# Kernel tuning notes

Measured on AMD Instinct MI355X. Metric: run time of the kernel, lower is better.

The kernel has to match this reference:

```python
import jax, jax.numpy as jnp
import numpy as np

B, N, F_IN, D = 4, 2048, 32, 64  # D = output_dim; gat1: heads=4, d=D//2=32; gat2: heads=1, d=D


def _gat(x, adj_norm, Wq, bq, Wk, bk, Wv, bv, heads, d):
    b, n, _ = x.shape
    q = (x @ Wq + bq).reshape(b, n, heads, d)
    k = (x @ Wk + bk).reshape(b, n, heads, d)
    v = (x @ Wv + bv).reshape(b, n, heads, d)
    scores = jnp.einsum('bihd,bjhd->bhij', q, k) / jnp.sqrt(jnp.float32(d))
    mask = jnp.where(adj_norm == 0, jnp.float32(-1e9), jnp.float32(0.0))  # [N,N]
    w = jax.nn.softmax(scores + mask[None, None], axis=-1)
    out = jnp.einsum('bhij,bjhd->bihd', w, v)
    return out.reshape(b, n, heads * d)


def setup_inputs() -> dict:
    key = jax.random.key(0)
    ks = jax.random.split(key, 12)
    s = 0.05
    x = jax.random.normal(ks[0], (B, N, F_IN), dtype=jnp.float32)
    adj = (jax.random.uniform(ks[1], (N, N)) < 0.02).astype(jnp.float32)  # sparse binary graph
    return {
        'x': x, 'adj': adj,
        'Wp': jax.random.normal(ks[2], (F_IN, D)) * s, 'bp': jnp.zeros((D,), jnp.float32),
        'Wq1': jax.random.normal(ks[3], (F_IN, 2 * D)) * s, 'bq1': jnp.zeros((2 * D,), jnp.float32),
        'Wk1': jax.random.normal(ks[4], (F_IN, 2 * D)) * s, 'bk1': jnp.zeros((2 * D,), jnp.float32),
        'Wv1': jax.random.normal(ks[5], (F_IN, 2 * D)) * s, 'bv1': jnp.zeros((2 * D,), jnp.float32),
        'Wq2': jax.random.normal(ks[6], (2 * D, D)) * s, 'bq2': jnp.zeros((D,), jnp.float32),
        'Wk2': jax.random.normal(ks[7], (2 * D, D)) * s, 'bk2': jnp.zeros((D,), jnp.float32),
        'Wv2': jax.random.normal(ks[8], (2 * D, D)) * s, 'bv2': jnp.zeros((D,), jnp.float32),
        'gamma': jnp.ones((D,), jnp.float32), 'beta': jnp.zeros((D,), jnp.float32),
    }


def reference(x, adj, Wp, bp, Wq1, bq1, Wk1, bk1, Wv1, bv1,
              Wq2, bq2, Wk2, bk2, Wv2, bv2, gamma, beta):
    # row-normalized adjacency (normalize_adjacency)
    adj_n = adj / (jnp.sum(adj, axis=1, keepdims=True) + 1e-6)
    proj = x @ Wp + bp                                   # [B,N,D]
    h = _gat(x, adj_n, Wq1, bq1, Wk1, bk1, Wv1, bv1, 4, D // 2)   # [B,N,2D]
    h = jax.nn.relu(h)                                   # dropout inactive (training=False)
    h = _gat(h, adj_n, Wq2, bq2, Wk2, bk2, Wv2, bv2, 1, D)        # [B,N,D]
    y = h + proj
    mu = jnp.mean(y, axis=-1, keepdims=True)
    var = jnp.var(y, axis=-1, keepdims=True)
    return gamma * (y - mu) / jnp.sqrt(var + 1e-6) + beta
```

## Files before the change

### kernel.cpp

```cpp
#include <hip/hip_runtime.h>
#include <hip/hip_bf16.h>

#define BB 4
#define NN 2048
#define FIN 32
#define DD 64
#define MAXDEG 256

__device__ __forceinline__ float bflo(unsigned u) { return __uint_as_float(u << 16); }
__device__ __forceinline__ float bfhi(unsigned u) { return __uint_as_float(u & 0xffff0000u); }
__device__ __forceinline__ float bf1(unsigned short s) { return __uint_as_float((unsigned)s << 16); }
__device__ __forceinline__ unsigned short f2bf(float f) {
    union { float f; unsigned u; } x; x.f = f;
    const unsigned r = x.u + 0x7fffu + ((x.u >> 16) & 1u);
    return (unsigned short)(r >> 16);
}

__global__ __launch_bounds__(128) void csr_gemm1(const float* __restrict__ adj,
    int* __restrict__ deg, int* __restrict__ col,
    const float* __restrict__ x,
    const float* __restrict__ Wp, const float* __restrict__ bp,
    const float* __restrict__ Wq, const float* __restrict__ bq,
    const float* __restrict__ Wk, const float* __restrict__ bk,
    const float* __restrict__ Wv, const float* __restrict__ bv,
    float* __restrict__ proj, float* __restrict__ q1,
    unsigned short* __restrict__ k1, unsigned short* __restrict__ v1) {
    const int bid = blockIdx.x;
    const int tid = threadIdx.x;

    if (bid < NN / 2) {
        const int lane = tid & 63;
        const int i = bid * 2 + (tid >> 6);
        const unsigned long long below = (1ull << lane) - 1ull;
        int base = 0;
        for (int j0 = 0; j0 < NN; j0 += 256) {
            const float4 a = *(const float4*)(adj + (size_t)i * NN + j0 + lane * 4);
            const bool n0 = a.x != 0.0f, n1 = a.y != 0.0f, n2 = a.z != 0.0f, n3 = a.w != 0.0f;
            const unsigned long long m0 = __ballot(n0);
            const unsigned long long m1 = __ballot(n1);
            const unsigned long long m2 = __ballot(n2);
            const unsigned long long m3 = __ballot(n3);
            int slot = base + __popcll(m0 & below) + __popcll(m1 & below)
                            + __popcll(m2 & below) + __popcll(m3 & below);
            const int jb = j0 + 4 * lane;
            if (n0) { if (slot < MAXDEG) col[i * MAXDEG + slot] = jb;     ++slot; }
            if (n1) { if (slot < MAXDEG) col[i * MAXDEG + slot] = jb + 1; ++slot; }
            if (n2) { if (slot < MAXDEG) col[i * MAXDEG + slot] = jb + 2; ++slot; }
            if (n3) { if (slot < MAXDEG) col[i * MAXDEG + slot] = jb + 3; ++slot; }
            base += __popcll(m0) + __popcll(m1) + __popcll(m2) + __popcll(m3);
        }
        if (lane == 0) deg[i] = base < MAXDEG ? base : MAXDEG;
        return;
    }

    const int r0 = (bid - NN / 2) * 4;
    __shared__ float xs[FIN * 4];
    {
        const int r = tid >> 5, k = tid & 31;
        xs[k * 4 + r] = x[(size_t)r0 * FIN + tid];
    }
    __syncthreads();

    float aq0 = bq[tid], aq1 = aq0, aq2 = aq0, aq3 = aq0;
    float ak0 = bk[tid], ak1 = ak0, ak2 = ak0, ak3 = ak0;
    float av0 = bv[tid], av1 = av0, av2 = av0, av3 = av0;
    #pragma unroll
    for (int k = 0; k < FIN; ++k) {
        const float wq = Wq[k * 128 + tid];
        const float wk = Wk[k * 128 + tid];
        const float wv = Wv[k * 128 + tid];
        const float4 xv = *(const float4*)&xs[k * 4];
        aq0 = fmaf(xv.x, wq, aq0); aq1 = fmaf(xv.y, wq, aq1);
        aq2 = fmaf(xv.z, wq, aq2); aq3 = fmaf(xv.w, wq, aq3);
        ak0 = fmaf(xv.x, wk, ak0); ak1 = fmaf(xv.y, wk, ak1);
        ak2 = fmaf(xv.z, wk, ak2); ak3 = fmaf(xv.w, wk, ak3);
        av0 = fmaf(xv.x, wv, av0); av1 = fmaf(xv.y, wv, av1);
        av2 = fmaf(xv.z, wv, av2); av3 = fmaf(xv.w, wv, av3);
    }
    q1[(size_t)(r0 + 0) * 128 + tid] = aq0; q1[(size_t)(r0 + 1) * 128 + tid] = aq1;
    q1[(size_t)(r0 + 2) * 128 + tid] = aq2; q1[(size_t)(r0 + 3) * 128 + tid] = aq3;
    k1[(size_t)(r0 + 0) * 128 + tid] = f2bf(ak0); k1[(size_t)(r0 + 1) * 128 + tid] = f2bf(ak1);
    k1[(size_t)(r0 + 2) * 128 + tid] = f2bf(ak2); k1[(size_t)(r0 + 3) * 128 + tid] = f2bf(ak3);
    v1[(size_t)(r0 + 0) * 128 + tid] = f2bf(av0); v1[(size_t)(r0 + 1) * 128 + tid] = f2bf(av1);
    v1[(size_t)(r0 + 2) * 128 + tid] = f2bf(av2); v1[(size_t)(r0 + 3) * 128 + tid] = f2bf(av3);

    if (tid < 64) {
        float a0 = bp[tid], a1 = a0, a2 = a0, a3 = a0;
        #pragma unroll
        for (int k = 0; k < FIN; ++k) {
            const float wp = Wp[k * 64 + tid];
            const float4 xv = *(const float4*)&xs[k * 4];
            a0 = fmaf(xv.x, wp, a0); a1 = fmaf(xv.y, wp, a1);
            a2 = fmaf(xv.z, wp, a2); a3 = fmaf(xv.w, wp, a3);
        }
        proj[(size_t)(r0 + 0) * 64 + tid] = a0; proj[(size_t)(r0 + 1) * 64 + tid] = a1;
        proj[(size_t)(r0 + 2) * 64 + tid] = a2; proj[(size_t)(r0 + 3) * 64 + tid] = a3;
    }
}

__global__ __launch_bounds__(192) void gemm2_fused(const unsigned short* __restrict__ h,
    const float* __restrict__ Wq, const float* __restrict__ bq,
    const float* __restrict__ Wk, const float* __restrict__ bk,
    const float* __restrict__ Wv, const float* __restrict__ bv,
    float* __restrict__ q2, unsigned short* __restrict__ k2,
    unsigned short* __restrict__ v2) {
    const int r0 = blockIdx.x * 8;
    const int tid = threadIdx.x;
    const int mat = tid / 64;
    const int c = tid & 63;
    __shared__ float xs[128][8];
    for (int idx = tid; idx < 8 * 128; idx += 192) {
        const int r = idx >> 7, k = idx & 127;
        xs[k][r] = bf1(h[(size_t)r0 * 128 + idx]);
    }
    __syncthreads();

    const float* __restrict__ W   = mat == 0 ? Wq : (mat == 1 ? Wk : Wv);
    const float* __restrict__ bia = mat == 0 ? bq : (mat == 1 ? bk : bv);

    float acc[8];
    const float b0 = bia[c];
    #pragma unroll
    for (int r = 0; r < 8; ++r) acc[r] = b0;
    #pragma unroll 4
    for (int k = 0; k < 128; ++k) {
        const float w = W[(size_t)k * 64 + c];
        const float4 xa = *(const float4*)&xs[k][0];
        const float4 xb = *(const float4*)&xs[k][4];
        acc[0] = fmaf(xa.x, w, acc[0]); acc[1] = fmaf(xa.y, w, acc[1]);
        acc[2] = fmaf(xa.z, w, acc[2]); acc[3] = fmaf(xa.w, w, acc[3]);
        acc[4] = fmaf(xb.x, w, acc[4]); acc[5] = fmaf(xb.y, w, acc[5]);
        acc[6] = fmaf(xb.z, w, acc[6]); acc[7] = fmaf(xb.w, w, acc[7]);
    }
    if (mat == 0) {
        #pragma unroll
        for (int r = 0; r < 8; ++r) q2[(size_t)(r0 + r) * 64 + c] = acc[r];
    } else {
        unsigned short* __restrict__ Yb = mat == 1 ? k2 : v2;
        #pragma unroll
        for (int r = 0; r < 8; ++r) Yb[(size_t)(r0 + r) * 64 + c] = f2bf(acc[r]);
    }
}

__device__ __forceinline__ void map_bi(int bid, int& b, int& i) {
    const int xcd = bid & 7;
    const int w = bid >> 3;
    b = xcd & 3;
    i = ((xcd >> 2) << 10) | w;
}

__global__ __launch_bounds__(128) void attn1_relu(const float* __restrict__ q1,
                                                  const unsigned short* __restrict__ k1,
                                                  const unsigned short* __restrict__ v1,
                                                  const int* __restrict__ deg,
                                                  const int* __restrict__ col,
                                                  unsigned short* __restrict__ h) {
    int b, i;
    map_bi(blockIdx.x, b, i);
    const int tid = threadIdx.x;

    __shared__ int nbr[MAXDEG];
    __shared__ float qs[128];
    __shared__ float ws[4 * MAXDEG];
    __shared__ int sdeg;

    const size_t stride = (size_t)NN * 128;
    if (tid == 0) sdeg = deg[i];
    qs[tid] = q1[(size_t)b * stride + (size_t)i * 128 + tid];
    __syncthreads();
    const int d = sdeg;
    for (int s = tid; s < d; s += 128) nbr[s] = col[i * MAXDEG + s];
    __syncthreads();

    const float scale = 0.17677669529663687f;
    const int hh = tid >> 5;
    const int t  = tid & 31;
    const int nr = (d + 31) >> 5;

    float qf[32];
    #pragma unroll
    for (int kk = 0; kk < 32; ++kk) qf[kk] = qs[hh * 32 + kk];

    float sc[8];
    for (int r = 0; r < nr; ++r) {
        const int idx = r * 32 + t;
        float s = -INFINITY;
        if (idx < d) {
            const int j = nbr[idx];
            const unsigned short* kr = k1 + (size_t)b * stride + (size_t)j * 128 + hh * 32;
            const uint4* kr4 = (const uint4*)kr;
            float acc0 = 0.0f, acc1 = 0.0f;
            #pragma unroll
            for (int w = 0; w < 4; w += 2) {
                const uint4 ka = kr4[w];
                const uint4 kb = kr4[w + 1];
                const float* qa = &qf[w * 8];
                const float* qb = &qf[w * 8 + 8];
                acc0 = fmaf(qa[0], bflo(ka.x), acc0); acc0 = fmaf(qa[1], bfhi(ka.x), acc0);
                acc0 = fmaf(qa[2], bflo(ka.y), acc0); acc0 = fmaf(qa[3], bfhi(ka.y), acc0);
                acc0 = fmaf(qa[4], bflo(ka.z), acc0); acc0 = fmaf(qa[5], bfhi(ka.z), acc0);
                acc0 = fmaf(qa[6], bflo(ka.w), acc0); acc0 = fmaf(qa[7], bfhi(ka.w), acc0);
                acc1 = fmaf(qb[0], bflo(kb.x), acc1); acc1 = fmaf(qb[1], bfhi(kb.x), acc1);
                acc1 = fmaf(qb[2], bflo(kb.y), acc1); acc1 = fmaf(qb[3], bfhi(kb.y), acc1);
                acc1 = fmaf(qb[4], bflo(kb.z), acc1); acc1 = fmaf(qb[5], bfhi(kb.z), acc1);
                acc1 = fmaf(qb[6], bflo(kb.w), acc1); acc1 = fmaf(qb[7], bfhi(kb.w), acc1);
            }
            s = (acc0 + acc1) * scale;
        }
        sc[r] = s;
    }

    float mx = sc[0];
    for (int r = 1; r < nr; ++r) mx = fmaxf(mx, sc[r]);
    #pragma unroll
    for (int off = 16; off >= 1; off >>= 1) mx = fmaxf(mx, __shfl_xor(mx, off));
    float se = 0.0f;
    for (int r = 0; r < nr; ++r) {
        const float e = __expf(sc[r] - mx);
        sc[r] = e;
        se += e;
    }
    #pragma unroll
    for (int off = 16; off >= 1; off >>= 1) se += __shfl_xor(se, off);
    const float inv = (d > 0) ? 1.0f / se : 0.0f;
    for (int r = 0; r < nr; ++r) {
        const int idx = r * 32 + t;
        if (idx < d) ws[hh * MAXDEG + idx] = sc[r] * inv;
    }
    __syncthreads();

    const int c = tid;
    const int h2 = c >> 5;
    const unsigned short* __restrict__ vb = v1 + (size_t)b * stride + c;
    const float* __restrict__ wp = ws + h2 * MAXDEG;
    float a0 = 0.0f, a1 = 0.0f, a2 = 0.0f, a3 = 0.0f;
    int t2 = 0;
    for (; t2 + 4 <= d; t2 += 4) {
        const int j0 = nbr[t2], j1 = nbr[t2 + 1], j2 = nbr[t2 + 2], j3 = nbr[t2 + 3];
        a0 = fmaf(wp[t2 + 0], bf1(vb[(size_t)j0 * 128]), a0);
        a1 = fmaf(wp[t2 + 1], bf1(vb[(size_t)j1 * 128]), a1);
        a2 = fmaf(wp[t2 + 2], bf1(vb[(size_t)j2 * 128]), a2);
        a3 = fmaf(wp[t2 + 3], bf1(vb[(size_t)j3 * 128]), a3);
    }
    for (; t2 < d; ++t2) a0 = fmaf(wp[t2], bf1(vb[(size_t)nbr[t2] * 128]), a0);
    float o = (a0 + a1) + (a2 + a3);
    if (d == 0) {
        float a = 0.0f;
        for (int j = 0; j < NN; ++j) a += bf1(vb[(size_t)j * 128]);
        o = a * (1.0f / NN);
    }
    h[(size_t)b * stride + (size_t)i * 128 + c] = f2bf(fmaxf(o, 0.0f));
}

__global__ __launch_bounds__(64) void attn2_ln(const float* __restrict__ q2,
                                               const unsigned short* __restrict__ k2,
                                               const unsigned short* __restrict__ v2,
                                               const float* __restrict__ proj,
                                               const int* __restrict__ deg,
                                               const int* __restrict__ col,
                                               const float* __restrict__ gamma,
                                               const float* __restrict__ beta,
                                               float* __restrict__ out) {
    int b, i;
    map_bi(blockIdx.x, b, i);
    const int lane = threadIdx.x;

    __shared__ int nbr[MAXDEG];
    __shared__ float qs[64];
    __shared__ float ws[MAXDEG];
    __shared__ int sdeg;

    const size_t stride = (size_t)NN * 64;
    if (lane == 0) sdeg = deg[i];
    qs[lane] = q2[(size_t)b * stride + (size_t)i * 64 + lane];
    __syncthreads();
    const int d = sdeg;
    for (int s = lane; s < d; s += 64) nbr[s] = col[i * MAXDEG + s];
    __syncthreads();

    const float scale = 0.125f;
    const int nr = (d + 63) >> 6;

    float sc[4];
    for (int r = 0; r < nr; ++r) {
        const int idx = r * 64 + lane;
        float s = -INFINITY;
        if (idx < d) {
            const int j = nbr[idx];
            const uint4* kr4 = (const uint4*)(k2 + (size_t)b * stride + (size_t)j * 64);
            float acc0 = 0.0f, acc1 = 0.0f;
            #pragma unroll
            for (int w = 0; w < 8; w += 2) {
                const uint4 ka = kr4[w];
                const uint4 kb = kr4[w + 1];
                const float4 qa0 = *(const float4*)&qs[w * 8];
                const float4 qa1 = *(const float4*)&qs[w * 8 + 4];
                const float4 qb0 = *(const float4*)&qs[w * 8 + 8];
                const float4 qb1 = *(const float4*)&qs[w * 8 + 12];
                acc0 = fmaf(qa0.x, bflo(ka.x), acc0); acc0 = fmaf(qa0.y, bfhi(ka.x), acc0);
                acc0 = fmaf(qa0.z, bflo(ka.y), acc0); acc0 = fmaf(qa0.w, bfhi(ka.y), acc0);
                acc0 = fmaf(qa1.x, bflo(ka.z), acc0); acc0 = fmaf(qa1.y, bfhi(ka.z), acc0);
                acc0 = fmaf(qa1.z, bflo(ka.w), acc0); acc0 = fmaf(qa1.w, bfhi(ka.w), acc0);
                acc1 = fmaf(qb0.x, bflo(kb.x), acc1); acc1 = fmaf(qb0.y, bfhi(kb.x), acc1);
                acc1 = fmaf(qb0.z, bflo(kb.y), acc1); acc1 = fmaf(qb0.w, bfhi(kb.y), acc1);
                acc1 = fmaf(qb1.x, bflo(kb.z), acc1); acc1 = fmaf(qb1.y, bfhi(kb.z), acc1);
                acc1 = fmaf(qb1.z, bflo(kb.w), acc1); acc1 = fmaf(qb1.w, bfhi(kb.w), acc1);
            }
            s = (acc0 + acc1) * scale;
        }
        sc[r] = s;
    }

    float mx = sc[0];
    for (int r = 1; r < nr; ++r) mx = fmaxf(mx, sc[r]);
    #pragma unroll
    for (int off = 32; off >= 1; off >>= 1) mx = fmaxf(mx, __shfl_xor(mx, off));
    float se = 0.0f;
    for (int r = 0; r < nr; ++r) {
        const float e = __expf(sc[r] - mx);
        sc[r] = e;
        se += e;
    }
    #pragma unroll
    for (int off = 32; off >= 1; off >>= 1) se += __shfl_xor(se, off);
    const float inv = (d > 0) ? 1.0f / se : 0.0f;
    for (int r = 0; r < nr; ++r) {
        const int idx = r * 64 + lane;
        if (idx < d) ws[idx] = sc[r] * inv;
    }
    __syncthreads();

    const unsigned short* __restrict__ vb = v2 + (size_t)b * stride + lane;
    float a0 = 0.0f, a1 = 0.0f, a2 = 0.0f, a3 = 0.0f;
    int t2 = 0;
    for (; t2 + 4 <= d; t2 += 4) {
        const int j0 = nbr[t2], j1 = nbr[t2 + 1], j2 = nbr[t2 + 2], j3 = nbr[t2 + 3];
        a0 = fmaf(ws[t2 + 0], bf1(vb[(size_t)j0 * 64]), a0);
        a1 = fmaf(ws[t2 + 1], bf1(vb[(size_t)j1 * 64]), a1);
        a2 = fmaf(ws[t2 + 2], bf1(vb[(size_t)j2 * 64]), a2);
        a3 = fmaf(ws[t2 + 3], bf1(vb[(size_t)j3 * 64]), a3);
    }
    for (; t2 < d; ++t2) a0 = fmaf(ws[t2], bf1(vb[(size_t)nbr[t2] * 64]), a0);
    float att = (a0 + a1) + (a2 + a3);
    if (d == 0) {
        float a = 0.0f;
        for (int j = 0; j < NN; ++j) a += bf1(vb[(size_t)j * 64]);
        att = a * (1.0f / NN);
    }

    const float y = att + proj[(size_t)b * stride + (size_t)i * 64 + lane];
    float s = y;
    s += __shfl_xor(s, 32); s += __shfl_xor(s, 16); s += __shfl_xor(s, 8);
    s += __shfl_xor(s, 4);  s += __shfl_xor(s, 2);  s += __shfl_xor(s, 1);
    const float mu = s * (1.0f / 64.0f);
    const float yc = y - mu;
    float sq = yc * yc;
    sq += __shfl_xor(sq, 32); sq += __shfl_xor(sq, 16); sq += __shfl_xor(sq, 8);
    sq += __shfl_xor(sq, 4);  sq += __shfl_xor(sq, 2);  sq += __shfl_xor(sq, 1);
    const float var = sq * (1.0f / 64.0f);
    out[(size_t)b * stride + (size_t)i * 64 + lane] =
        gamma[lane] * yc * rsqrtf(var + 1e-6f) + beta[lane];
}

extern "C" void kernel_launch(void* const* d_in, const int* in_sizes, int n_in,
                              void* d_out, int out_size, void* d_ws, size_t ws_size,
                              hipStream_t stream) {
    const float* x     = (const float*)d_in[0];
    const float* adj   = (const float*)d_in[1];
    const float* Wp    = (const float*)d_in[2];
    const float* bp    = (const float*)d_in[3];
    const float* Wq1   = (const float*)d_in[4];
    const float* bq1   = (const float*)d_in[5];
    const float* Wk1   = (const float*)d_in[6];
    const float* bk1   = (const float*)d_in[7];
    const float* Wv1   = (const float*)d_in[8];
    const float* bv1   = (const float*)d_in[9];
    const float* Wq2   = (const float*)d_in[10];
    const float* bq2   = (const float*)d_in[11];
    const float* Wk2   = (const float*)d_in[12];
    const float* bk2   = (const float*)d_in[13];
    const float* Wv2   = (const float*)d_in[14];
    const float* bv2   = (const float*)d_in[15];
    const float* gamma = (const float*)d_in[16];
    const float* beta  = (const float*)d_in[17];
    float* out = (float*)d_out;

    char* ws = (char*)d_ws;
    size_t off = 0;
    auto alloc = [&](size_t bytes) {
        void* p = ws + off;
        off = (off + bytes + 255) & ~(size_t)255;
        return p;
    };
    int*            deg  = (int*)           alloc((size_t)NN * 4);
    int*            col  = (int*)           alloc((size_t)NN * MAXDEG * 4);
    float*          proj = (float*)         alloc((size_t)BB * NN * 64 * 4);
    float*          q1   = (float*)         alloc((size_t)BB * NN * 128 * 4);
    unsigned short* k1   = (unsigned short*)alloc((size_t)BB * NN * 128 * 2);
    unsigned short* v1   = (unsigned short*)alloc((size_t)BB * NN * 128 * 2);
    unsigned short* h    = (unsigned short*)alloc((size_t)BB * NN * 128 * 2);
    float*          q2   = (float*)         alloc((size_t)BB * NN * 64 * 4);
    unsigned short* k2   = (unsigned short*)alloc((size_t)BB * NN * 64 * 2);
    unsigned short* v2   = (unsigned short*)alloc((size_t)BB * NN * 64 * 2);

    csr_gemm1<<<NN / 2 + BB * NN / 4, 128, 0, stream>>>(
        adj, deg, col, x, Wp, bp, Wq1, bq1, Wk1, bk1, Wv1, bv1, proj, q1, k1, v1);

    attn1_relu<<<BB * NN, 128, 0, stream>>>(q1, k1, v1, deg, col, h);

    gemm2_fused<<<BB * NN / 8, 192, 0, stream>>>(h, Wq2, bq2, Wk2, bk2, Wv2, bv2,
                                                 q2, k2, v2);

    attn2_ln<<<BB * NN, 64, 0, stream>>>(q2, k2, v2, proj, deg, col, gamma, beta, out);
}
```

Before: 71.34 us.

## Switch intermediates to fp16 with packed half2 dot products and paired value loads

All intermediate Q/K/V and hidden tensors move from bf16/fp32 to fp16. Query-key dot products now use packed __hfma2 instead of scalar fp32 FMAs. The value aggregation loops load half2 pairs, with each thread covering two columns and the neighbor loop split across wave groups that are reduced through LDS or shuffles. This trims memory traffic and instruction count in the attention kernels, at the cost of fp16 range and accumulation precision in the score sums plus an extra reduction step.

```diff
diff --git a/kernel.cpp b/kernel.cpp
--- a/kernel.cpp
+++ b/kernel.cpp
@@ -1,5 +1,6 @@
 #include <hip/hip_runtime.h>
 #include <hip/hip_bf16.h>
+#include <hip/hip_fp16.h>
 
 #define BB 4
 #define NN 2048
@@ -7,13 +8,8 @@
 #define DD 64
 #define MAXDEG 256
 
-__device__ __forceinline__ float bflo(unsigned u) { return __uint_as_float(u << 16); }
-__device__ __forceinline__ float bfhi(unsigned u) { return __uint_as_float(u & 0xffff0000u); }
-__device__ __forceinline__ float bf1(unsigned short s) { return __uint_as_float((unsigned)s << 16); }
-__device__ __forceinline__ unsigned short f2bf(float f) {
-    union { float f; unsigned u; } x; x.f = f;
-    const unsigned r = x.u + 0x7fffu + ((x.u >> 16) & 1u);
-    return (unsigned short)(r >> 16);
+__device__ __forceinline__ __half2 u2h2(unsigned u) {
+    union { unsigned u; __half2 h; } x; x.u = u; return x.h;
 }
 
 __global__ __launch_bounds__(128) void csr_gemm1(const float* __restrict__ adj,
@@ -23,8 +19,8 @@
     const float* __restrict__ Wq, const float* __restrict__ bq,
     const float* __restrict__ Wk, const float* __restrict__ bk,
     const float* __restrict__ Wv, const float* __restrict__ bv,
-    float* __restrict__ proj, float* __restrict__ q1,
-    unsigned short* __restrict__ k1, unsigned short* __restrict__ v1) {
+    float* __restrict__ proj, __half* __restrict__ q1,
+    __half* __restrict__ k1, __half* __restrict__ v1) {
     const int bid = blockIdx.x;
     const int tid = threadIdx.x;
 
@@ -77,12 +73,18 @@
         av0 = fmaf(xv.x, wv, av0); av1 = fmaf(xv.y, wv, av1);
         av2 = fmaf(xv.z, wv, av2); av3 = fmaf(xv.w, wv, av3);
     }
-    q1[(size_t)(r0 + 0) * 128 + tid] = aq0; q1[(size_t)(r0 + 1) * 128 + tid] = aq1;
-    q1[(size_t)(r0 + 2) * 128 + tid] = aq2; q1[(size_t)(r0 + 3) * 128 + tid] = aq3;
-    k1[(size_t)(r0 + 0) * 128 + tid] = f2bf(ak0); k1[(size_t)(r0 + 1) * 128 + tid] = f2bf(ak1);
-    k1[(size_t)(r0 + 2) * 128 + tid] = f2bf(ak2); k1[(size_t)(r0 + 3) * 128 + tid] = f2bf(ak3);
-    v1[(size_t)(r0 + 0) * 128 + tid] = f2bf(av0); v1[(size_t)(r0 + 1) * 128 + tid] = f2bf(av1);
-    v1[(size_t)(r0 + 2) * 128 + tid] = f2bf(av2); v1[(size_t)(r0 + 3) * 128 + tid] = f2bf(av3);
+    q1[(size_t)(r0 + 0) * 128 + tid] = __float2half_rn(aq0);
+    q1[(size_t)(r0 + 1) * 128 + tid] = __float2half_rn(aq1);
+    q1[(size_t)(r0 + 2) * 128 + tid] = __float2half_rn(aq2);
+    q1[(size_t)(r0 + 3) * 128 + tid] = __float2half_rn(aq3);
+    k1[(size_t)(r0 + 0) * 128 + tid] = __float2half_rn(ak0);
+    k1[(size_t)(r0 + 1) * 128 + tid] = __float2half_rn(ak1);
+    k1[(size_t)(r0 + 2) * 128 + tid] = __float2half_rn(ak2);
+    k1[(size_t)(r0 + 3) * 128 + tid] = __float2half_rn(ak3);
+    v1[(size_t)(r0 + 0) * 128 + tid] = __float2half_rn(av0);
+    v1[(size_t)(r0 + 1) * 128 + tid] = __float2half_rn(av1);
+    v1[(size_t)(r0 + 2) * 128 + tid] = __float2half_rn(av2);
+    v1[(size_t)(r0 + 3) * 128 + tid] = __float2half_rn(av3);
 
     if (tid < 64) {
         float a0 = bp[tid], a1 = a0, a2 = a0, a3 = a0;
@@ -98,25 +100,27 @@
     }
 }
 
-__global__ __launch_bounds__(192) void gemm2_fused(const unsigned short* __restrict__ h,
+__global__ __launch_bounds__(192) void gemm2_fused(const __half* __restrict__ h,
     const float* __restrict__ Wq, const float* __restrict__ bq,
     const float* __restrict__ Wk, const float* __restrict__ bk,
     const float* __restrict__ Wv, const float* __restrict__ bv,
-    float* __restrict__ q2, unsigned short* __restrict__ k2,
-    unsigned short* __restrict__ v2) {
+    __half* __restrict__ q2, __half* __restrict__ k2, __half* __restrict__ v2) {
     const int r0 = blockIdx.x * 8;
     const int tid = threadIdx.x;
     const int mat = tid / 64;
     const int c = tid & 63;
     __shared__ float xs[128][8];
-    for (int idx = tid; idx < 8 * 128; idx += 192) {
-        const int r = idx >> 7, k = idx & 127;
-        xs[k][r] = bf1(h[(size_t)r0 * 128 + idx]);
+    for (int idx = tid; idx < 512; idx += 192) {
+        const __half2 hv = ((const __half2*)(h + (size_t)r0 * 128))[idx];
+        const int flat = idx * 2;
+        const int r = flat >> 7, k = flat & 127;
+        xs[k][r] = __low2float(hv); xs[k + 1][r] = __high2float(hv);
     }
     __syncthreads();
 
     const float* __restrict__ W   = mat == 0 ? Wq : (mat == 1 ? Wk : Wv);
     const float* __restrict__ bia = mat == 0 ? bq : (mat == 1 ? bk : bv);
+    __half* __restrict__ Y        = mat == 0 ? q2 : (mat == 1 ? k2 : v2);
 
     float acc[8];
     const float b0 = bia[c];
@@ -132,14 +136,8 @@
         acc[4] = fmaf(xb.x, w, acc[4]); acc[5] = fmaf(xb.y, w, acc[5]);
         acc[6] = fmaf(xb.z, w, acc[6]); acc[7] = fmaf(xb.w, w, acc[7]);
     }
-    if (mat == 0) {
-        #pragma unroll
-        for (int r = 0; r < 8; ++r) q2[(size_t)(r0 + r) * 64 + c] = acc[r];
-    } else {
-        unsigned short* __restrict__ Yb = mat == 1 ? k2 : v2;
-        #pragma unroll
-        for (int r = 0; r < 8; ++r) Yb[(size_t)(r0 + r) * 64 + c] = f2bf(acc[r]);
-    }
+    #pragma unroll
+    for (int r = 0; r < 8; ++r) Y[(size_t)(r0 + r) * 64 + c] = __float2half_rn(acc[r]);
 }
 
 __device__ __forceinline__ void map_bi(int bid, int& b, int& i) {
@@ -149,24 +147,25 @@
     i = ((xcd >> 2) << 10) | w;
 }
 
-__global__ __launch_bounds__(128) void attn1_relu(const float* __restrict__ q1,
-                                                  const unsigned short* __restrict__ k1,
-                                                  const unsigned short* __restrict__ v1,
+__global__ __launch_bounds__(128) void attn1_relu(const __half* __restrict__ q1,
+                                                  const __half* __restrict__ k1,
+                                                  const __half* __restrict__ v1,
                                                   const int* __restrict__ deg,
                                                   const int* __restrict__ col,
-                                                  unsigned short* __restrict__ h) {
+                                                  __half* __restrict__ h) {
     int b, i;
     map_bi(blockIdx.x, b, i);
     const int tid = threadIdx.x;
 
     __shared__ int nbr[MAXDEG];
-    __shared__ float qs[128];
-    __shared__ float ws[4 * MAXDEG];
+    __shared__ __half2 qs2[64];
+    __shared__ float wsA[4 * MAXDEG];
+    __shared__ float2 part[2][64];
     __shared__ int sdeg;
 
     const size_t stride = (size_t)NN * 128;
     if (tid == 0) sdeg = deg[i];
-    qs[tid] = q1[(size_t)b * stride + (size_t)i * 128 + tid];
+    if (tid < 64) qs2[tid] = ((const __half2*)(q1 + (size_t)b * stride + (size_t)i * 128))[tid];
     __syncthreads();
     const int d = sdeg;
     for (int s = tid; s < d; s += 128) nbr[s] = col[i * MAXDEG + s];
@@ -177,9 +176,9 @@
     const int t  = tid & 31;
     const int nr = (d + 31) >> 5;
 
-    float qf[32];
-    #pragma unroll
-    for (int kk = 0; kk < 32; ++kk) qf[kk] = qs[hh * 32 + kk];
+    __half2 qh2[16];
+    #pragma unroll
+    for (int w = 0; w < 16; ++w) qh2[w] = qs2[hh * 16 + w];
 
     float sc[8];
     for (int r = 0; r < nr; ++r) {
@@ -187,25 +186,18 @@
         float s = -INFINITY;
         if (idx < d) {
             const int j = nbr[idx];
-            const unsigned short* kr = k1 + (size_t)b * stride + (size_t)j * 128 + hh * 32;
-            const uint4* kr4 = (const uint4*)kr;
-            float acc0 = 0.0f, acc1 = 0.0f;
+            const uint4* kr4 = (const uint4*)(k1 + (size_t)b * stride + (size_t)j * 128 + hh * 32);
+            __half2 a2 = __float2half2_rn(0.0f), b2 = __float2half2_rn(0.0f);
             #pragma unroll
-            for (int w = 0; w < 4; w += 2) {
-                const uint4 ka = kr4[w];
-                const uint4 kb = kr4[w + 1];
-                const float* qa = &qf[w * 8];
-                const float* qb = &qf[w * 8 + 8];
-                acc0 = fmaf(qa[0], bflo(ka.x), acc0); acc0 = fmaf(qa[1], bfhi(ka.x), acc0);
-                acc0 = fmaf(qa[2], bflo(ka.y), acc0); acc0 = fmaf(qa[3], bfhi(ka.y), acc0);
-                acc0 = fmaf(qa[4], bflo(ka.z), acc0); acc0 = fmaf(qa[5], bfhi(ka.z), acc0);
-                acc0 = fmaf(qa[6], bflo(ka.w), acc0); acc0 = fmaf(qa[7], bfhi(ka.w), acc0);
-                acc1 = fmaf(qb[0], bflo(kb.x), acc1); acc1 = fmaf(qb[1], bfhi(kb.x), acc1);
-                acc1 = fmaf(qb[2], bflo(kb.y), acc1); acc1 = fmaf(qb[3], bfhi(kb.y), acc1);
-                acc1 = fmaf(qb[4], bflo(kb.z), acc1); acc1 = fmaf(qb[5], bfhi(kb.z), acc1);
-                acc1 = fmaf(qb[6], bflo(kb.w), acc1); acc1 = fmaf(qb[7], bfhi(kb.w), acc1);
+            for (int w = 0; w < 4; ++w) {
+                const uint4 kw = kr4[w];
+                a2 = __hfma2(qh2[w * 4 + 0], u2h2(kw.x), a2);
+                b2 = __hfma2(qh2[w * 4 + 1], u2h2(kw.y), b2);
+                a2 = __hfma2(qh2[w * 4 + 2], u2h2(kw.z), a2);
+                b2 = __hfma2(qh2[w * 4 + 3], u2h2(kw.w), b2);
             }
-            s = (acc0 + acc1) * scale;
+            s = ((__low2float(a2) + __high2float(a2)) +
+                 (__low2float(b2) + __high2float(b2))) * scale;
         }
         sc[r] = s;
     }
@@ -225,36 +217,55 @@
     const float inv = (d > 0) ? 1.0f / se : 0.0f;
     for (int r = 0; r < nr; ++r) {
         const int idx = r * 32 + t;
-        if (idx < d) ws[hh * MAXDEG + idx] = sc[r] * inv;
-    }
-    __syncthreads();
-
-    const int c = tid;
-    const int h2 = c >> 5;
-    const unsigned short* __restrict__ vb = v1 + (size_t)b * stride + c;
-    const float* __restrict__ wp = ws + h2 * MAXDEG;
-    float a0 = 0.0f, a1 = 0.0f, a2 = 0.0f, a3 = 0.0f;
-    int t2 = 0;
-    for (; t2 + 4 <= d; t2 += 4) {
-        const int j0 = nbr[t2], j1 = nbr[t2 + 1], j2 = nbr[t2 + 2], j3 = nbr[t2 + 3];
-        a0 = fmaf(wp[t2 + 0], bf1(vb[(size_t)j0 * 128]), a0);
-        a1 = fmaf(wp[t2 + 1], bf1(vb[(size_t)j1 * 128]), a1);
-        a2 = fmaf(wp[t2 + 2], bf1(vb[(size_t)j2 * 128]), a2);
-        a3 = fmaf(wp[t2 + 3], bf1(vb[(size_t)j3 * 128]), a3);
-    }
-    for (; t2 < d; ++t2) a0 = fmaf(wp[t2], bf1(vb[(size_t)nbr[t2] * 128]), a0);
-    float o = (a0 + a1) + (a2 + a3);
-    if (d == 0) {
-        float a = 0.0f;
-        for (int j = 0; j < NN; ++j) a += bf1(vb[(size_t)j * 128]);
-        o = a * (1.0f / NN);
-    }
-    h[(size_t)b * stride + (size_t)i * 128 + c] = f2bf(fmaxf(o, 0.0f));
-}
-
-__global__ __launch_bounds__(64) void attn2_ln(const float* __restrict__ q2,
-                                               const unsigned short* __restrict__ k2,
-                                               const unsigned short* __restrict__ v2,
+        if (idx < d) wsA[hh * MAXDEG + idx] = sc[r] * inv;
+    }
+    __syncthreads();
+
+    const int wv = tid >> 6;
+    const int l  = tid & 63;
+    const int hB = l >> 4;
+    const __half* __restrict__ vrow = v1 + (size_t)b * stride + 2 * l;
+    const float* __restrict__ wp = wsA + hB * MAXDEG;
+    float a0 = 0.0f, a1 = 0.0f, b0 = 0.0f, b1 = 0.0f;
+    int t2 = wv;
+    for (; t2 + 2 < d; t2 += 4) {
+        const int ja = nbr[t2], jb = nbr[t2 + 2];
+        const __half2 va = u2h2(*(const unsigned*)(vrow + (size_t)ja * 128));
+        const __half2 vb = u2h2(*(const unsigned*)(vrow + (size_t)jb * 128));
+        const float wa = wp[t2], wb = wp[t2 + 2];
+        a0 = fmaf(wa, __low2float(va), a0); a1 = fmaf(wa, __high2float(va), a1);
+        b0 = fmaf(wb, __low2float(vb), b0); b1 = fmaf(wb, __high2float(vb), b1);
+    }
+    if (t2 < d) {
+        const int ja = nbr[t2];
+        const __half2 va = u2h2(*(const unsigned*)(vrow + (size_t)ja * 128));
+        const float wa = wp[t2];
+        a0 = fmaf(wa, __low2float(va), a0); a1 = fmaf(wa, __high2float(va), a1);
+    }
+    part[wv][l] = make_float2(a0 + b0, a1 + b1);
+    __syncthreads();
+
+    if (tid < 64) {
+        float o0 = part[0][tid].x + part[1][tid].x;
+        float o1 = part[0][tid].y + part[1][tid].y;
+        if (d == 0) {
+            float s0 = 0.0f, s1 = 0.0f;
+            const __half* vr = v1 + (size_t)b * stride + 2 * tid;
+            for (int j = 0; j < NN; ++j) {
+                const __half2 vj = u2h2(*(const unsigned*)(vr + (size_t)j * 128));
+                s0 += __low2float(vj); s1 += __high2float(vj);
+            }
+            o0 = s0 * (1.0f / NN); o1 = s1 * (1.0f / NN);
+        }
+        o0 = fmaxf(o0, 0.0f); o1 = fmaxf(o1, 0.0f);
+        ((__half2*)(h + (size_t)b * stride + (size_t)i * 128))[tid] =
+            __halves2half2(__float2half_rn(o0), __float2half_rn(o1));
+    }
+}
+
+__global__ __launch_bounds__(64) void attn2_ln(const __half* __restrict__ q2,
+                                               const __half* __restrict__ k2,
+                                               const __half* __restrict__ v2,
                                                const float* __restrict__ proj,
                                                const int* __restrict__ deg,
                                                const int* __restrict__ col,
@@ -266,13 +277,14 @@
     const int lane = threadIdx.x;
 
     __shared__ int nbr[MAXDEG];
-    __shared__ float qs[64];
-    __shared__ float ws[MAXDEG];
+    __shared__ __half2 qs2[32];
+    __shared__ float wsA[MAXDEG];
+    __shared__ float att_lds[64];
     __shared__ int sdeg;
 
     const size_t stride = (size_t)NN * 64;
     if (lane == 0) sdeg = deg[i];
-    qs[lane] = q2[(size_t)b * stride + (size_t)i * 64 + lane];
+    if (lane < 32) qs2[lane] = ((const __half2*)(q2 + (size_t)b * stride + (size_t)i * 64))[lane];
     __syncthreads();
     const int d = sdeg;
     for (int s = lane; s < d; s += 64) nbr[s] = col[i * MAXDEG + s];
@@ -280,6 +292,10 @@
 
     const float scale = 0.125f;
     const int nr = (d + 63) >> 6;
+
+    __half2 qh2[32];
+    #pragma unroll
+    for (int w = 0; w < 32; ++w) qh2[w] = qs2[w];
 
     float sc[4];
     for (int r = 0; r < nr; ++r) {
@@ -288,25 +304,17 @@
         if (idx < d) {
             const int j = nbr[idx];
             const uint4* kr4 = (const uint4*)(k2 + (size_t)b * stride + (size_t)j * 64);
-            float acc0 = 0.0f, acc1 = 0.0f;
+            __half2 a2 = __float2half2_rn(0.0f), b2 = __float2half2_rn(0.0f);
             #pragma unroll
-            for (int w = 0; w < 8; w += 2) {
-                const uint4 ka = kr4[w];
-                const uint4 kb = kr4[w + 1];
-                const float4 qa0 = *(const float4*)&qs[w * 8];
-                const float4 qa1 = *(const float4*)&qs[w * 8 + 4];
-                const float4 qb0 = *(const float4*)&qs[w * 8 + 8];
-                const float4 qb1 = *(const float4*)&qs[w * 8 + 12];
-                acc0 = fmaf(qa0.x, bflo(ka.x), acc0); acc0 = fmaf(qa0.y, bfhi(ka.x), acc0);
-                acc0 = fmaf(qa0.z, bflo(ka.y), acc0); acc0 = fmaf(qa0.w, bfhi(ka.y), acc0);
-                acc0 = fmaf(qa1.x, bflo(ka.z), acc0); acc0 = fmaf(qa1.y, bfhi(ka.z), acc0);
-                acc0 = fmaf(qa1.z, bflo(ka.w), acc0); acc0 = fmaf(qa1.w, bfhi(ka.w), acc0);
-                acc1 = fmaf(qb0.x, bflo(kb.x), acc1); acc1 = fmaf(qb0.y, bfhi(kb.x), acc1);
-                acc1 = fmaf(qb0.z, bflo(kb.y), acc1); acc1 = fmaf(qb0.w, bfhi(kb.y), acc1);
-                acc1 = fmaf(qb1.x, bflo(kb.z), acc1); acc1 = fmaf(qb1.y, bfhi(kb.z), acc1);
-                acc1 = fmaf(qb1.z, bflo(kb.w), acc1); acc1 = fmaf(qb1.w, bfhi(kb.w), acc1);
+            for (int w = 0; w < 8; ++w) {
+                const uint4 kw = kr4[w];
+                a2 = __hfma2(qh2[w * 4 + 0], u2h2(kw.x), a2);
+                b2 = __hfma2(qh2[w * 4 + 1], u2h2(kw.y), b2);
+                a2 = __hfma2(qh2[w * 4 + 2], u2h2(kw.z), a2);
+                b2 = __hfma2(qh2[w * 4 + 3], u2h2(kw.w), b2);
             }
-            s = (acc0 + acc1) * scale;
+            s = ((__low2float(a2) + __high2float(a2)) +
+                 (__low2float(b2) + __high2float(b2))) * scale;
         }
         sc[r] = s;
     }
@@ -326,25 +334,38 @@
     const float inv = (d > 0) ? 1.0f / se : 0.0f;
     for (int r = 0; r < nr; ++r) {
         const int idx = r * 64 + lane;
-        if (idx < d) ws[idx] = sc[r] * inv;
-    }
-    __syncthreads();
-
-    const unsigned short* __restrict__ vb = v2 + (size_t)b * stride + lane;
-    float a0 = 0.0f, a1 = 0.0f, a2 = 0.0f, a3 = 0.0f;
-    int t2 = 0;
-    for (; t2 + 4 <= d; t2 += 4) {
-        const int j0 = nbr[t2], j1 = nbr[t2 + 1], j2 = nbr[t2 + 2], j3 = nbr[t2 + 3];
-        a0 = fmaf(ws[t2 + 0], bf1(vb[(size_t)j0 * 64]), a0);
-        a1 = fmaf(ws[t2 + 1], bf1(vb[(size_t)j1 * 64]), a1);
-        a2 = fmaf(ws[t2 + 2], bf1(vb[(size_t)j2 * 64]), a2);
-        a3 = fmaf(ws[t2 + 3], bf1(vb[(size_t)j3 * 64]), a3);
-    }
-    for (; t2 < d; ++t2) a0 = fmaf(ws[t2], bf1(vb[(size_t)nbr[t2] * 64]), a0);
-    float att = (a0 + a1) + (a2 + a3);
+        if (idx < d) wsA[idx] = sc[r] * inv;
+    }
+    __syncthreads();
+
+    const int p = lane & 31, g = lane >> 5;
+    const __half* __restrict__ vrow = v2 + (size_t)b * stride + 2 * p;
+    float a0 = 0.0f, a1 = 0.0f, b0 = 0.0f, b1 = 0.0f;
+    int t2 = g;
+    for (; t2 + 2 < d; t2 += 4) {
+        const int ja = nbr[t2], jb = nbr[t2 + 2];
+        const __half2 va = u2h2(*(const unsigned*)(vrow + (size_t)ja * 64));
+        const __half2 vb = u2h2(*(const unsigned*)(vrow + (size_t)jb * 64));
+        const float wa = wsA[t2], wb = wsA[t2 + 2];
+        a0 = fmaf(wa, __low2float(va), a0); a1 = fmaf(wa, __high2float(va), a1);
+        b0 = fmaf(wb, __low2float(vb), b0); b1 = fmaf(wb, __high2float(vb), b1);
+    }
+    if (t2 < d) {
+        const int ja = nbr[t2];
+        const __half2 va = u2h2(*(const unsigned*)(vrow + (size_t)ja * 64));
+        const float wa = wsA[t2];
+        a0 = fmaf(wa, __low2float(va), a0); a1 = fmaf(wa, __high2float(va), a1);
+    }
+    a0 += b0; a1 += b1;
+    a0 += __shfl_xor(a0, 32);
+    a1 += __shfl_xor(a1, 32);
+    if (g == 0) { att_lds[2 * p] = a0; att_lds[2 * p + 1] = a1; }
+    __syncthreads();
+    float att = att_lds[lane];
     if (d == 0) {
         float a = 0.0f;
-        for (int j = 0; j < NN; ++j) a += bf1(vb[(size_t)j * 64]);
+        const __half* vr = v2 + (size_t)b * stride + lane;
+        for (int j = 0; j < NN; ++j) a += __half2float(vr[(size_t)j * 64]);
         att = a * (1.0f / NN);
     }
 
@@ -392,16 +413,16 @@
         off = (off + bytes + 255) & ~(size_t)255;
         return p;
     };
-    int*            deg  = (int*)           alloc((size_t)NN * 4);
-    int*            col  = (int*)           alloc((size_t)NN * MAXDEG * 4);
-    float*          proj = (float*)         alloc((size_t)BB * NN * 64 * 4);
-    float*          q1   = (float*)         alloc((size_t)BB * NN * 128 * 4);
-    unsigned short* k1   = (unsigned short*)alloc((size_t)BB * NN * 128 * 2);
-    unsigned short* v1   = (unsigned short*)alloc((size_t)BB * NN * 128 * 2);
-    unsigned short* h    = (unsigned short*)alloc((size_t)BB * NN * 128 * 2);
-    float*          q2   = (float*)         alloc((size_t)BB * NN * 64 * 4);
-    unsigned short* k2   = (unsigned short*)alloc((size_t)BB * NN * 64 * 2);
-    unsigned short* v2   = (unsigned short*)alloc((size_t)BB * NN * 64 * 2);
+    int*    deg  = (int*)   alloc((size_t)NN * 4);
+    int*    col  = (int*)   alloc((size_t)NN * MAXDEG * 4);
+    float*  proj = (float*) alloc((size_t)BB * NN * 64 * 4);
+    __half* q1   = (__half*)alloc((size_t)BB * NN * 128 * 2);
+    __half* k1   = (__half*)alloc((size_t)BB * NN * 128 * 2);
+    __half* v1   = (__half*)alloc((size_t)BB * NN * 128 * 2);
+    __half* h    = (__half*)alloc((size_t)BB * NN * 128 * 2);
+    __half* q2   = (__half*)alloc((size_t)BB * NN * 64 * 2);
+    __half* k2   = (__half*)alloc((size_t)BB * NN * 64 * 2);
+    __half* v2   = (__half*)alloc((size_t)BB * NN * 64 * 2);
 
     csr_gemm1<<<NN / 2 + BB * NN / 4, 128, 0, stream>>>(
         adj, deg, col, x, Wp, bp, Wq1, bq1, Wk1, bk1, Wv1, bv1, proj, q1, k1, v1);
```

New measurement: 66.23 us. -7.2%, faster.
